# Kernel tuning notes

Measured on AMD Instinct MI355X. Metric: run time of the kernel, lower is better.

## Reference

```python
import jax, jax.numpy as jnp
import numpy as np
import math
from jax import lax


def _conv(x, w, b, stride=1, pad=0, groups=1):
    # x: [B,C,H,W], w: [O, C//groups, kh, kw] (OIHW)
    out = lax.conv_general_dilated(x, w, (stride, stride), [(pad, pad), (pad, pad)],
                                   feature_group_count=groups,
                                   dimension_numbers=('NCHW', 'OIHW', 'NCHW'))
    return out + b.reshape(1, -1, 1, 1)


def _shared_conv(x, k2d, b, stride=1, pad=0):
    # SharedConv: one [k,k] kernel shared across all channels (depthwise), scalar bias
    C = x.shape[1]
    w = jnp.broadcast_to(k2d[None, None], (C, 1) + k2d.shape)
    out = lax.conv_general_dilated(x, w, (stride, stride), [(pad, pad), (pad, pad)],
                                   feature_group_count=C,
                                   dimension_numbers=('NCHW', 'OIHW', 'NCHW'))
    return out + b


def _bn(x, g, b, m, v, eps=1e-5):
    scale = (g / jnp.sqrt(v + eps)).reshape(1, -1, 1, 1)
    return (x - m.reshape(1, -1, 1, 1)) * scale + b.reshape(1, -1, 1, 1)


def _leaky(x, s=0.01):
    return jnp.where(x >= 0, x, s * x)


def _max_leaky(x, t, s):
    # cap values above threshold with leaky slope
    return jnp.where(x <= t, x, t + s * (x - t))


def _min_leaky(x, t, s):
    # cap values below threshold with leaky slope
    return jnp.where(x >= t, x, t + s * (x - t))


def _mode_pool(x, k=11, padding=1):
    # histogram mode pooling: 17 bins over quantized values, stride 1
    xp = jnp.pad(x, ((0, 0), (0, 0), (padding, padding), (padding, padding)))
    bins = jnp.clip(jnp.round(xp * 16.0), 0.0, 16.0).astype(jnp.int32)
    oh = jax.nn.one_hot(bins, 17, dtype=x.dtype)           # [B,C,Hp,Wp,17]
    counts = lax.reduce_window(oh, 0.0, lax.add, (1, 1, k, k, 1), (1, 1, 1, 1, 1), 'VALID')
    return jnp.argmax(counts, axis=-1).astype(x.dtype) / 16.0


def _emphase(x, w, k=11):
    # EmphaseLocal: unsharp-style local emphasis with per-channel learnable scale
    s = lax.reduce_window(x, 0.0, lax.add, (1, 1, k, k), (1, 1, 1, 1), 'SAME')
    avg = s / float(k * k)
    return x + w.reshape(1, -1, 1, 1) * (x - avg)


def setup_inputs() -> dict:
    key = jax.random.key(0)
    ks = jax.random.split(key, 20)
    f32 = jnp.float32
    B, Cin, H, W = 2, 3, 512, 512
    C2 = 64  # half_out_channels * 2
    return {
        'x': jax.random.uniform(ks[0], (B, Cin, H, W), f32),
        'w1': jax.random.normal(ks[1], (C2, Cin, 1, 1), f32) * 0.1,
        'b1': jax.random.normal(ks[2], (C2,), f32) * 0.05,
        'w2': jax.random.normal(ks[3], (C2, 2, 1, 1), f32) * 0.1,  # groups=32
        'b2': jax.random.normal(ks[4], (C2,), f32) * 0.05,
        'down_k': jax.random.normal(ks[5], (3, 3), f32) * 0.1,
        'down_b': jax.random.normal(ks[6], (), f32) * 0.05,
        'ft_gamma': 1.0 + jax.random.normal(ks[7], (C2,), f32) * 0.1,
        'ft_beta': jax.random.normal(ks[8], (C2,), f32) * 0.05,
        'ft_mean': jax.random.normal(ks[9], (C2,), f32) * 0.05,
        'ft_var': jax.random.uniform(ks[10], (C2,), f32, 0.5, 1.5),
        'ft_k': jax.random.normal(ks[11], (1, 1), f32) * 0.5 + 1.0,
        'ft_b': jax.random.normal(ks[12], (), f32) * 0.05,
        'emph_w': jax.random.normal(ks[13], (C2,), f32) * 0.1,
        'interp_k': jax.random.normal(ks[14], (5, 5), f32) * 0.1,
        'interp_b': jax.random.normal(ks[15], (), f32) * 0.05,
        'i_gamma': 1.0 + jax.random.normal(ks[16], (C2,), f32) * 0.1,
        'i_beta': jax.random.normal(ks[17], (C2,), f32) * 0.05,
        'i_mean': jax.random.normal(ks[18], (C2,), f32) * 0.05,
        'i_var': jax.random.uniform(ks[19], (C2,), f32, 0.5, 1.5),
    }


def reference(x, w1, b1, w2, b2, down_k, down_b,
              ft_gamma, ft_beta, ft_mean, ft_var, ft_k, ft_b, emph_w,
              interp_k, interp_b, i_gamma, i_beta, i_mean, i_var):
    B, _, H, W = x.shape
    C2 = w1.shape[0]
    # prepare: ColorDownsample(16) -> ModePool2d(11,1,1) -> 1x1 conv -> MaxLeakyReLU -> grouped 1x1 conv -> MinLeakyReLU
    xd = jnp.round(x * 255.0 / 16.0) * 16.0 / 256.0
    h = _mode_pool(xd, k=11, padding=1)                 # [B,Cin,H-8,W-8]
    h = _max_leaky(_conv(h, w1, b1), 0.1, 0.01)
    groups = C2 // w2.shape[1]
    d = _min_leaky(_conv(h, w2, b2, groups=groups), 0.1, 0.01)
    score = jnp.zeros((B, C2, H, W), x.dtype)
    n = math.floor(math.log(min(d.shape[2], d.shape[3]), 3))
    for _ in range(n):
        # downgrade: shared 3x3 stride-3 conv + leaky
        d = _leaky(_shared_conv(d, down_k, down_b, stride=3, pad=1))
        # zoom back to full resolution, then interpolate branch (shared 5x5 conv + BN + leaky)
        z = jax.image.resize(d, (B, C2, H, W), method='bilinear')
        z = _bn(_shared_conv(z, interp_k, interp_b, pad=2), i_gamma, i_beta, i_mean, i_var)
        score = score + _leaky(z)
    # ft applied 3 times with shared weights: BN -> shared 1x1 conv -> EmphaseLocal
    for _ in range(3):
        s = _bn(score, ft_gamma, ft_beta, ft_mean, ft_var)
        s = _shared_conv(s, ft_k, ft_b)
        score = _emphase(s, emph_w, k=11)
    return score
```

## Files before the change

### kernel.cpp

```cpp
#include <hip/hip_runtime.h>

#define NB 2
#define CIN 3
#define HH 512
#define WW 512
#define C2 64
#define HM 504

typedef float v2f  __attribute__((ext_vector_type(2)));
typedef float v2fu __attribute__((ext_vector_type(2), aligned(4)));

__global__ __launch_bounds__(256) void k_mode(const float* __restrict__ x,
                                              unsigned char* __restrict__ hmode) {
  __shared__ unsigned char tile[26 * 26];
  int bc  = blockIdx.z;
  int ty0 = blockIdx.y * 16, tx0 = blockIdx.x * 16;
  const float* src = x + (size_t)bc * HH * WW;
  for (int i = threadIdx.x; i < 26 * 26; i += 256) {
    int r = i / 26, cl = i % 26;
    int Y = ty0 + r, X = tx0 + cl;
    unsigned char v = 0;
    if (Y >= 1 && Y <= HH && X >= 1 && X <= WW) {
      float val = src[(Y - 1) * WW + (X - 1)];
      float q = rintf((val * 255.0f) / 16.0f);
      q = fminf(fmaxf(q, 0.0f), 16.0f);
      v = (unsigned char)(int)q;
    }
    tile[i] = v;
  }
  __syncthreads();
  int ty = threadIdx.x >> 4, tx = threadIdx.x & 15;
  int oy = ty0 + ty, ox = tx0 + tx;
  if (oy >= HM || ox >= HM) return;
  unsigned long long w0 = 0, w1 = 0, w2 = 0;
  for (int dy = 0; dy < 11; dy++) {
    #pragma unroll
    for (int dx = 0; dx < 11; dx++) {
      int b = tile[(ty + dy) * 26 + tx + dx];
      unsigned long long inc = 1ull << ((b & 7) * 8);
      if (b < 8) w0 += inc;
      else if (b < 16) w1 += inc;
      else w2 += inc;
    }
  }
  int best = -1, bestb = 0;
  #pragma unroll
  for (int b = 0; b < 17; b++) {
    int cnt;
    if (b < 8)       cnt = (int)((w0 >> (b * 8)) & 0xff);
    else if (b < 16) cnt = (int)((w1 >> ((b - 8) * 8)) & 0xff);
    else             cnt = (int)(w2 & 0xff);
    if (cnt > best) { best = cnt; bestb = b; }
  }
  hmode[bc * HM * HM + oy * HM + ox] = (unsigned char)bestb;
}

__global__ __launch_bounds__(256) void k_prepare(const unsigned char* __restrict__ hmode,
                                                 const float* __restrict__ w1,
                                                 const float* __restrict__ b1,
                                                 const float* __restrict__ w2,
                                                 const float* __restrict__ b2,
                                                 const float* __restrict__ down_k,
                                                 const float* __restrict__ down_b,
                                                 float* __restrict__ d1) {
  int bc = blockIdx.y;
  int b  = bc >> 6;
  int c  = bc & 63;
  int pix = blockIdx.x * 256 + threadIdx.x;
  if (pix >= 168 * 168) return;
  int oy = pix / 168, ox = pix % 168;
  int c0 = (c >> 1) << 1;
  float w1a0 = w1[c0 * 3], w1a1 = w1[c0 * 3 + 1], w1a2 = w1[c0 * 3 + 2], b1a = b1[c0];
  float w1b0 = w1[(c0 + 1) * 3], w1b1 = w1[(c0 + 1) * 3 + 1], w1b2 = w1[(c0 + 1) * 3 + 2], b1b = b1[c0 + 1];
  float w2a = w2[c * 2], w2b = w2[c * 2 + 1], b2c = b2[c];
  float kb = *down_b;
  const unsigned char* h0p = hmode + (b * 3 + 0) * HM * HM;
  const unsigned char* h1p = hmode + (b * 3 + 1) * HM * HM;
  const unsigned char* h2p = hmode + (b * 3 + 2) * HM * HM;
  float acc = 0.0f;
  #pragma unroll
  for (int ky = 0; ky < 3; ky++) {
    int y = 3 * oy - 1 + ky;
    if (y < 0 || y >= HM) continue;
    #pragma unroll
    for (int kx = 0; kx < 3; kx++) {
      int xx = 3 * ox - 1 + kx;
      if (xx < 0 || xx >= HM) continue;
      int o = y * HM + xx;
      float hh0 = h0p[o] * (1.0f / 16.0f);
      float hh1 = h1p[o] * (1.0f / 16.0f);
      float hh2 = h2p[o] * (1.0f / 16.0f);
      float a0 = w1a0 * hh0 + w1a1 * hh1 + w1a2 * hh2 + b1a;
      float a1 = w1b0 * hh0 + w1b1 * hh1 + w1b2 * hh2 + b1b;
      a0 = (a0 <= 0.1f) ? a0 : 0.1f + 0.01f * (a0 - 0.1f);
      a1 = (a1 <= 0.1f) ? a1 : 0.1f + 0.01f * (a1 - 0.1f);
      float v = w2a * a0 + w2b * a1 + b2c;
      v = (v >= 0.1f) ? v : 0.1f + 0.01f * (v - 0.1f);
      acc += down_k[ky * 3 + kx] * v;
    }
  }
  float r = acc + kb;
  r = (r >= 0.0f) ? r : 0.01f * r;
  d1[bc * 168 * 168 + pix] = r;
}

__global__ __launch_bounds__(256) void k_down(const float* __restrict__ din,
                                              float* __restrict__ dout,
                                              const float* __restrict__ down_k,
                                              const float* __restrict__ down_b,
                                              int S, int So) {
  int bc = blockIdx.y;
  int pix = blockIdx.x * 256 + threadIdx.x;
  if (pix >= So * So) return;
  int oy = pix / So, ox = pix % So;
  const float* p = din + bc * S * S;
  float acc = 0.0f;
  #pragma unroll
  for (int ky = 0; ky < 3; ky++) {
    int y = 3 * oy - 1 + ky;
    if (y < 0 || y >= S) continue;
    #pragma unroll
    for (int kx = 0; kx < 3; kx++) {
      int xx = 3 * ox - 1 + kx;
      if (xx < 0 || xx >= S) continue;
      acc += down_k[ky * 3 + kx] * p[y * S + xx];
    }
  }
  float r = acc + *down_b;
  r = (r >= 0.0f) ? r : 0.01f * r;
  dout[bc * So * So + pix] = r;
}

__global__ __launch_bounds__(256) void k_lut(float2* __restrict__ lutpk) {
  int idx = blockIdx.x * 256 + threadIdx.x;
  if (idx >= 5 * 512) return;
  int lvl = idx >> 9, Y = idx & 511;
  const int Ls[5] = {168, 56, 19, 7, 3};
  int L = Ls[lvl];
  float f = (Y + 0.5f) * ((float)L / 512.0f) - 0.5f;
  f = fminf(fmaxf(f, 0.0f), (float)(L - 1));
  int y0 = (int)f;
  float w = f - (float)y0;
  lutpk[idx] = make_float2(__int_as_float(y0), w);
}

__global__ __launch_bounds__(256, 4) void k_score(const float* __restrict__ d1,
                                                  const float* __restrict__ d2,
                                                  const float* __restrict__ d3,
                                                  const float* __restrict__ d4,
                                                  const float* __restrict__ d5,
                                                  const float2* __restrict__ lutpk,
                                                  const float* __restrict__ interp_k,
                                                  const float* __restrict__ interp_b,
                                                  const float* __restrict__ i_gamma,
                                                  const float* __restrict__ i_beta,
                                                  const float* __restrict__ i_mean,
                                                  const float* __restrict__ i_var,
                                                  float* __restrict__ score) {
  __shared__ float xrow[24 * 68];
  __shared__ float kap[64 * 20];
  __shared__ int   abase[64];

  int bc = blockIdx.y;
  int c  = bc & 63;
  int tile = blockIdx.x;
  int tyi = tile >> 3, txi = tile & 7;
  int ty0 = tyi * 64, tx0 = txi * 64;
  float K[25];
  #pragma unroll
  for (int i = 0; i < 25; i++)
    K[i] = __int_as_float(__builtin_amdgcn_readfirstlane(__float_as_int(interp_k[i])));
  float ib  = __int_as_float(__builtin_amdgcn_readfirstlane(__float_as_int(*interp_b)));
  float isc = i_gamma[c] * rsqrtf(i_var[c] + 1e-5f);
  float ibe = i_beta[c] - i_mean[c] * isc;
  int tid = threadIdx.x;
  int oyl = (tid >> 4) << 2, oxl = (tid & 15) << 2;
  float acc[4][4];
  #pragma unroll
  for (int i = 0; i < 4; i++)
    #pragma unroll
    for (int j = 0; j < 4; j++) acc[i][j] = 0.0f;

  const float* dls[5] = {d1, d2, d3, d4, d5};
  const int Ls[5]  = {168, 56, 19, 7, 3};
  const int RLs[5] = {24, 10, 5, 3, 3};

  auto fillLevel = [&](int l) {
    int L = Ls[l], RR = RLs[l];
    const float* dp = dls[l] + bc * L * L;
    const float2* lp = lutpk + (l << 9);
    int Ylo = max(ty0 - 2, 0);
    int r0 = __float_as_int(lp[Ylo].x);
    {
      int y = tid >> 2, rr = tid & 3;
      int Y = ty0 + y;
      float kv0 = 0.0f, kv1 = 0.0f, kv2 = 0.0f, kv3 = 0.0f, kv4 = 0.0f;
      int ab = -1;
      #pragma unroll
      for (int ky = 0; ky < 5; ky++) {
        int yy = Y + ky - 2;
        if (yy >= 0 && yy < 512) {
          float2 pk = lp[yy];
          int a0 = __float_as_int(pk.x);
          float wv = pk.y;
          if (ab < 0) ab = a0;
          float cf = 0.0f;
          if (a0 - ab == rr)     cf += 1.0f - wv;
          if (a0 + 1 - ab == rr) cf += wv;
          kv0 += cf * K[ky * 5 + 0];
          kv1 += cf * K[ky * 5 + 1];
          kv2 += cf * K[ky * 5 + 2];
          kv3 += cf * K[ky * 5 + 3];
          kv4 += cf * K[ky * 5 + 4];
        }
      }
      float* kp = &kap[y * 20 + rr * 5];
      kp[0] = kv0; kp[1] = kv1; kp[2] = kv2; kp[3] = kv3; kp[4] = kv4;
      if (rr == 0) abase[y] = ab - r0;
    }
    for (int i = tid; i < RR * 68; i += 256) {
      int r = i / 68, xx = i - r * 68;
      int X = tx0 - 2 + xx;
      float v = 0.0f;
      if (X >= 0 && X < 512) {
        float2 pk = lp[X];
        int ix = __float_as_int(pk.x);
        float wx = pk.y;
        int gr = min(r0 + r, L - 1);
        const float* rp = dp + gr * L + ix;
        float v0 = rp[0], v1 = rp[1];
        v = v0 + wx * (v1 - v0);
      }
      xrow[r * 68 + xx] = v;
    }
  };

  auto convAcc = [&](int rspan, int rlim) {
    #pragma unroll
    for (int i = 0; i < 4; i++) {
      int y = oyl + i;
      int ab = abase[y];
      float t0 = 0.0f, t1 = 0.0f, t2v = 0.0f, t3 = 0.0f;
      for (int rr = 0; rr < rspan; rr++) {
        int row = min(ab + rr, rlim);
        const float* xp = &xrow[row * 68 + oxl];
        float4 A = *(const float4*)xp;
        float4 B = *(const float4*)(xp + 4);
        const float* kp = &kap[y * 20 + rr * 5];
        float k0 = kp[0], k1 = kp[1], k2 = kp[2], k3 = kp[3], k4 = kp[4];
        t0  += k0 * A.x + k1 * A.y + k2 * A.z + k3 * A.w + k4 * B.x;
        t1  += k0 * A.y + k1 * A.z + k2 * A.w + k3 * B.x + k4 * B.y;
        t2v += k0 * A.z + k1 * A.w + k2 * B.x + k3 * B.y + k4 * B.z;
        t3  += k0 * A.w + k1 * B.x + k2 * B.y + k3 * B.z + k4 * B.w;
      }
      float tv[4] = {t0, t1, t2v, t3};
      #pragma unroll
      for (int j = 0; j < 4; j++) {
        float v = (tv[j] + ib) * isc + ibe;
        v = (v >= 0.0f) ? v : 0.01f * v;
        acc[i][j] += v;
      }
    }
  };

  #pragma unroll 1
  for (int l = 0; l < 5; l++) {
    if (l) __syncthreads();
    fillLevel(l);
    __syncthreads();
    if (l == 0) convAcc(4, RLs[0] - 1);
    else        convAcc(3, RLs[l] - 1);
  }

  float* op = score + bc * 512 * 512;
  #pragma unroll
  for (int i = 0; i < 4; i++) {
    int Y = ty0 + oyl + i;
    float4 vv = make_float4(acc[i][0], acc[i][1], acc[i][2], acc[i][3]);
    *(float4*)(op + Y * 512 + tx0 + oxl) = vv;
  }
}

__global__ __launch_bounds__(256, 2) void k_ft_pipe(const float* __restrict__ s_in,
                                                    float* __restrict__ s_out,
                                                    const float* __restrict__ ft_gamma,
                                                    const float* __restrict__ ft_beta,
                                                    const float* __restrict__ ft_mean,
                                                    const float* __restrict__ ft_var,
                                                    const float* __restrict__ ft_k,
                                                    const float* __restrict__ ft_b,
                                                    const float* __restrict__ emph_w) {
  __shared__ float ring2[12 * 512];
  __shared__ float ring3[12 * 512];
  __shared__ float brow1[528];
  __shared__ float brow2[528];
  __shared__ float brow3[528];

  const int bc = blockIdx.y;
  const int c  = bc & 63;
  const int R0 = blockIdx.x << 7;
  const int mstart = R0 - 15;

  const float sc  = ft_gamma[c] * rsqrtf(ft_var[c] + 1e-5f);
  const float fk = *ft_k, fb = *ft_b;
  const float Aff = sc * fk;
  const float Cc  = (ft_beta[c] - ft_mean[c] * sc) * fk + fb;
  const float w   = emph_w[c];
  const float opw = 1.0f + w;
  const float okw = w * (1.0f / 121.0f);

  const int tid = threadIdx.x;
  const int x0  = tid << 1;

  const float* sp = s_in + ((size_t)bc << 18) + x0;
  float*       op = s_out + ((size_t)bc << 18) + x0;

  if (tid < 12) {
    int p = (tid < 6) ? tid : (512 + tid);
    brow1[p] = 0.0f; brow2[p] = 0.0f; brow3[p] = 0.0f;
  }

  auto ldraw = [&](int row) -> v2f {
    int rc = min(max(row, 0), 511);
    return *(const v2f*)(sp + ((size_t)rc << 9));
  };

  auto rowsum = [&](const float* b) -> v2f {
    const float* p = b + x0;
    v2f w0 = *(const v2f*)(p);
    v2f w1 = *(const v2f*)(p + 2);
    v2f w2 = *(const v2f*)(p + 4);
    v2f w3 = *(const v2f*)(p + 6);
    v2f w4 = *(const v2f*)(p + 8);
    v2f w5 = *(const v2f*)(p + 10);
    v2f w6 = *(const v2f*)(p + 12);
    float smid = ((w1.x + w1.y) + (w2.x + w2.y)) +
                 ((w3.x + w3.y) + (w4.x + w4.y)) + (w5.x + w5.y);
    v2f r;
    r.x = smid + w0.y;
    r.y = smid + w6.x;
    return r;
  };

  v2f cs1 = (v2f)0.0f, cs2 = (v2f)0.0f, cs3 = (v2f)0.0f;
  v2f out1p = (v2f)0.0f, out2p = (v2f)0.0f;

  int m = mstart;
  v2f gf = ldraw(m);
  v2f go = ldraw(m - 11);
  v2f gc = ldraw(m - 5);
  int sw = 0;

  #pragma unroll 1
  for (int i = 0; i < 160; ++i, ++m) {
    v2f gf_n = ldraw(m + 1);
    v2f go_n = ldraw(m - 10);
    v2f gc_n = ldraw(m - 4);

    int swn = (sw + 1 == 12) ? 0 : sw + 1;
    int swc = (sw + 7 >= 12) ? sw - 5 : sw + 7;

    {
      v2f u1f = (m >= 0 && m < 512) ? (gf * Aff + Cc) : (v2f)0.0f;
      int r = m - 11;
      v2f u1o = (r >= mstart && r >= 0 && r < 512) ? (go * Aff + Cc) : (v2f)0.0f;
      cs1 += u1f - u1o;
      *(v2f*)(brow1 + 6 + x0) = cs1;
    }
    {
      v2f u2s = out1p * Aff + Cc;
      *(v2f*)(ring2 + sw * 512 + x0) = u2s;
      int rf = m - 6;
      v2f u2f = (rf >= 0 && rf < 512) ? u2s : (v2f)0.0f;
      int r = m - 17;
      v2f u2or = *(const v2f*)(ring2 + swn * 512 + x0);
      v2f u2o = (r >= mstart - 6 && r >= 0 && r < 512) ? u2or : (v2f)0.0f;
      cs2 += u2f - u2o;
      *(v2f*)(brow2 + 6 + x0) = cs2;
    }
    {
      v2f u3s = out2p * Aff + Cc;
      *(v2f*)(ring3 + sw * 512 + x0) = u3s;
      int rf = m - 12;
      v2f u3f = (rf >= 0 && rf < 512) ? u3s : (v2f)0.0f;
      int r = m - 23;
      v2f u3or = *(const v2f*)(ring3 + swn * 512 + x0);
      v2f u3o = (r >= mstart - 12 && r >= 0 && r < 512) ? u3or : (v2f)0.0f;
      cs3 += u3f - u3o;
      *(v2f*)(brow3 + 6 + x0) = cs3;
    }
    __syncthreads();
    {
      int rc1 = m - 5;
      v2f u1c = (rc1 >= 0 && rc1 < 512) ? (gc * Aff + Cc) : (v2f)0.0f;
      v2f B1 = rowsum(brow1);
      out1p = u1c * opw - B1 * okw;
    }
    {
      int rc2 = m - 11;
      v2f u2cr = *(const v2f*)(ring2 + swc * 512 + x0);
      v2f u2c = (rc2 >= mstart - 6 && rc2 >= 0 && rc2 < 512) ? u2cr : (v2f)0.0f;
      v2f B2 = rowsum(brow2);
      out2p = u2c * opw - B2 * okw;
    }
    {
      int rc3 = m - 17;
      v2f u3cr = *(const v2f*)(ring3 + swc * 512 + x0);
      v2f u3c = (rc3 >= mstart - 12 && rc3 >= 0 && rc3 < 512) ? u3cr : (v2f)0.0f;
      v2f B3 = rowsum(brow3);
      v2f o3 = u3c * opw - B3 * okw;
      if (i >= 32)
        *(v2f*)(op + ((size_t)(m - 17) << 9)) = o3;
    }
    __syncthreads();
    gf = gf_n; go = go_n; gc = gc_n;
    sw = swn;
  }
}

extern "C" void kernel_launch(void* const* d_in, const int* in_sizes, int n_in,
                              void* d_out, int out_size, void* d_ws, size_t ws_size,
                              hipStream_t stream) {
  const float* x        = (const float*)d_in[0];
  const float* w1       = (const float*)d_in[1];
  const float* b1       = (const float*)d_in[2];
  const float* w2       = (const float*)d_in[3];
  const float* b2       = (const float*)d_in[4];
  const float* down_k   = (const float*)d_in[5];
  const float* down_b   = (const float*)d_in[6];
  const float* ft_gamma = (const float*)d_in[7];
  const float* ft_beta  = (const float*)d_in[8];
  const float* ft_mean  = (const float*)d_in[9];
  const float* ft_var   = (const float*)d_in[10];
  const float* ft_k     = (const float*)d_in[11];
  const float* ft_b     = (const float*)d_in[12];
  const float* emph_w   = (const float*)d_in[13];
  const float* interp_k = (const float*)d_in[14];
  const float* interp_b = (const float*)d_in[15];
  const float* i_gamma  = (const float*)d_in[16];
  const float* i_beta   = (const float*)d_in[17];
  const float* i_mean   = (const float*)d_in[18];
  const float* i_var    = (const float*)d_in[19];
  float* out = (float*)d_out;

  char* ws = (char*)d_ws;
  size_t off = 0;
  auto alloc = [&](size_t bytes) { size_t r = off; off += (bytes + 255) & ~(size_t)255; return r; };
  unsigned char* hmode = (unsigned char*)(ws + alloc((size_t)NB * CIN * HM * HM));
  float* d1 = (float*)(ws + alloc((size_t)NB * C2 * 168 * 168 * 4));
  float* d2 = (float*)(ws + alloc((size_t)NB * C2 * 56 * 56 * 4));
  float* d3 = (float*)(ws + alloc((size_t)NB * C2 * 19 * 19 * 4));
  float* d4 = (float*)(ws + alloc((size_t)NB * C2 * 7 * 7 * 4));
  float* d5 = (float*)(ws + alloc((size_t)NB * C2 * 3 * 3 * 4));
  float* s0 = (float*)(ws + alloc((size_t)NB * C2 * 512 * 512 * 4));
  float2* lutpk = (float2*)(ws + alloc((size_t)5 * 512 * 8));

  k_mode<<<dim3(32, 32, NB * CIN), 256, 0, stream>>>(x, hmode);
  k_lut<<<10, 256, 0, stream>>>(lutpk);
  k_prepare<<<dim3((168 * 168 + 255) / 256, NB * C2), 256, 0, stream>>>(
      hmode, w1, b1, w2, b2, down_k, down_b, d1);
  k_down<<<dim3((56 * 56 + 255) / 256, NB * C2), 256, 0, stream>>>(d1, d2, down_k, down_b, 168, 56);
  k_down<<<dim3((19 * 19 + 255) / 256, NB * C2), 256, 0, stream>>>(d2, d3, down_k, down_b, 56, 19);
  k_down<<<dim3((7 * 7 + 255) / 256, NB * C2), 256, 0, stream>>>(d3, d4, down_k, down_b, 19, 7);
  k_down<<<dim3((3 * 3 + 255) / 256, NB * C2), 256, 0, stream>>>(d4, d5, down_k, down_b, 7, 3);
  k_score<<<dim3(64, NB * C2), 256, 0, stream>>>(d1, d2, d3, d4, d5, lutpk,
                                                 interp_k, interp_b,
                                                 i_gamma, i_beta, i_mean, i_var, s0);
  k_ft_pipe<<<dim3(4, NB * C2), 256, 0, stream>>>(s0, out, ft_gamma, ft_beta, ft_mean,
                                                  ft_var, ft_k, ft_b, emph_w);
}
```

Baseline: 576.6 us.

## Move ft ring buffers to registers and double-buffer row sums to drop a barrier

The fused three-pass ft kernel now keeps its 12-row delay rings in per-thread registers through a 12-way unrolled loop instead of shared memory. The row-sum staging buffers are double-buffered, which removes the second __syncthreads per row, and the forward global load is prefetched two rows ahead. Shared memory use shrinks, so launch bounds ask for 3 blocks per CU. The trade-off is more registers and code size, and the loop now runs 168 iterations instead of 160, with extra iterations that do not store. Register pressure under the higher occupancy target could cause spills.

After: 549.5 us. 4.7% less time.

```diff
diff --git a/kernel.cpp b/kernel.cpp
--- a/kernel.cpp
+++ b/kernel.cpp
@@ -281,7 +281,7 @@
   }
 }
 
-__global__ __launch_bounds__(256, 2) void k_ft_pipe(const float* __restrict__ s_in,
+__global__ __launch_bounds__(256, 3) void k_ft_pipe(const float* __restrict__ s_in,
                                                     float* __restrict__ s_out,
                                                     const float* __restrict__ ft_gamma,
                                                     const float* __restrict__ ft_beta,
@@ -290,11 +290,9 @@
                                                     const float* __restrict__ ft_k,
                                                     const float* __restrict__ ft_b,
                                                     const float* __restrict__ emph_w) {
-  __shared__ float ring2[12 * 512];
-  __shared__ float ring3[12 * 512];
-  __shared__ float brow1[528];
-  __shared__ float brow2[528];
-  __shared__ float brow3[528];
+  __shared__ float brow1[2][524];
+  __shared__ float brow2[2][524];
+  __shared__ float brow3[2][524];
 
   const int bc = blockIdx.y;
   const int c  = bc & 63;
@@ -315,9 +313,11 @@
   const float* sp = s_in + ((size_t)bc << 18) + x0;
   float*       op = s_out + ((size_t)bc << 18) + x0;
 
-  if (tid < 12) {
-    int p = (tid < 6) ? tid : (512 + tid);
-    brow1[p] = 0.0f; brow2[p] = 0.0f; brow3[p] = 0.0f;
+  if (tid < 72) {
+    int a = tid / 24, pb = (tid / 12) & 1, e = tid % 12;
+    int idx = (e < 6) ? e : (512 + e);
+    float* base = (a == 0) ? &brow1[pb][0] : (a == 1) ? &brow2[pb][0] : &brow3[pb][0];
+    base[idx] = 0.0f;
   }
 
   auto ldraw = [&](int row) -> v2f {
@@ -345,76 +345,81 @@
   v2f cs1 = (v2f)0.0f, cs2 = (v2f)0.0f, cs3 = (v2f)0.0f;
   v2f out1p = (v2f)0.0f, out2p = (v2f)0.0f;
 
-  int m = mstart;
-  v2f gf = ldraw(m);
-  v2f go = ldraw(m - 11);
-  v2f gc = ldraw(m - 5);
-  int sw = 0;
+  v2f r2[12], r3[12];
+  #pragma unroll
+  for (int k = 0; k < 12; k++) { r2[k] = (v2f)0.0f; r3[k] = (v2f)0.0f; }
+
+  v2f gf  = ldraw(mstart);
+  v2f gfa = ldraw(mstart + 1);
+  v2f go  = ldraw(mstart - 11);
+  v2f gc  = ldraw(mstart - 5);
 
   #pragma unroll 1
-  for (int i = 0; i < 160; ++i, ++m) {
-    v2f gf_n = ldraw(m + 1);
-    v2f go_n = ldraw(m - 10);
-    v2f gc_n = ldraw(m - 4);
-
-    int swn = (sw + 1 == 12) ? 0 : sw + 1;
-    int swc = (sw + 7 >= 12) ? sw - 5 : sw + 7;
-
-    {
-      v2f u1f = (m >= 0 && m < 512) ? (gf * Aff + Cc) : (v2f)0.0f;
-      int r = m - 11;
-      v2f u1o = (r >= mstart && r >= 0 && r < 512) ? (go * Aff + Cc) : (v2f)0.0f;
-      cs1 += u1f - u1o;
-      *(v2f*)(brow1 + 6 + x0) = cs1;
-    }
-    {
-      v2f u2s = out1p * Aff + Cc;
-      *(v2f*)(ring2 + sw * 512 + x0) = u2s;
-      int rf = m - 6;
-      v2f u2f = (rf >= 0 && rf < 512) ? u2s : (v2f)0.0f;
-      int r = m - 17;
-      v2f u2or = *(const v2f*)(ring2 + swn * 512 + x0);
-      v2f u2o = (r >= mstart - 6 && r >= 0 && r < 512) ? u2or : (v2f)0.0f;
-      cs2 += u2f - u2o;
-      *(v2f*)(brow2 + 6 + x0) = cs2;
-    }
-    {
-      v2f u3s = out2p * Aff + Cc;
-      *(v2f*)(ring3 + sw * 512 + x0) = u3s;
-      int rf = m - 12;
-      v2f u3f = (rf >= 0 && rf < 512) ? u3s : (v2f)0.0f;
-      int r = m - 23;
-      v2f u3or = *(const v2f*)(ring3 + swn * 512 + x0);
-      v2f u3o = (r >= mstart - 12 && r >= 0 && r < 512) ? u3or : (v2f)0.0f;
-      cs3 += u3f - u3o;
-      *(v2f*)(brow3 + 6 + x0) = cs3;
-    }
-    __syncthreads();
-    {
-      int rc1 = m - 5;
-      v2f u1c = (rc1 >= 0 && rc1 < 512) ? (gc * Aff + Cc) : (v2f)0.0f;
-      v2f B1 = rowsum(brow1);
-      out1p = u1c * opw - B1 * okw;
-    }
-    {
-      int rc2 = m - 11;
-      v2f u2cr = *(const v2f*)(ring2 + swc * 512 + x0);
-      v2f u2c = (rc2 >= mstart - 6 && rc2 >= 0 && rc2 < 512) ? u2cr : (v2f)0.0f;
-      v2f B2 = rowsum(brow2);
-      out2p = u2c * opw - B2 * okw;
-    }
-    {
-      int rc3 = m - 17;
-      v2f u3cr = *(const v2f*)(ring3 + swc * 512 + x0);
-      v2f u3c = (rc3 >= mstart - 12 && rc3 >= 0 && rc3 < 512) ? u3cr : (v2f)0.0f;
-      v2f B3 = rowsum(brow3);
-      v2f o3 = u3c * opw - B3 * okw;
-      if (i >= 32)
-        *(v2f*)(op + ((size_t)(m - 17) << 9)) = o3;
-    }
-    __syncthreads();
-    gf = gf_n; go = go_n; gc = gc_n;
-    sw = swn;
+  for (int ii = 0; ii < 14; ++ii) {
+    #pragma unroll
+    for (int j = 0; j < 12; ++j) {
+      const int i = ii * 12 + j;
+      const int m = mstart + i;
+      v2f gf_n2 = ldraw(m + 2);
+      v2f go_n  = ldraw(m - 10);
+      v2f gc_n  = ldraw(m - 4);
+
+      const int p = j & 1;
+
+      {
+        v2f u1f = (m >= 0 && m < 512) ? (gf * Aff + Cc) : (v2f)0.0f;
+        int r = m - 11;
+        v2f u1o = (r >= mstart && r >= 0 && r < 512) ? (go * Aff + Cc) : (v2f)0.0f;
+        cs1 += u1f - u1o;
+        *(v2f*)(&brow1[p][6 + x0]) = cs1;
+      }
+      {
+        v2f u2s = out1p * Aff + Cc;
+        v2f u2or = r2[(j + 1) % 12];
+        r2[j] = u2s;
+        int rf = m - 6;
+        v2f u2f = (rf >= 0 && rf < 512) ? u2s : (v2f)0.0f;
+        int r = m - 17;
+        v2f u2o = (r >= mstart - 6 && r >= 0 && r < 512) ? u2or : (v2f)0.0f;
+        cs2 += u2f - u2o;
+        *(v2f*)(&brow2[p][6 + x0]) = cs2;
+      }
+      {
+        v2f u3s = out2p * Aff + Cc;
+        v2f u3or = r3[(j + 1) % 12];
+        r3[j] = u3s;
+        int rf = m - 12;
+        v2f u3f = (rf >= 0 && rf < 512) ? u3s : (v2f)0.0f;
+        int r = m - 23;
+        v2f u3o = (r >= mstart - 12 && r >= 0 && r < 512) ? u3or : (v2f)0.0f;
+        cs3 += u3f - u3o;
+        *(v2f*)(&brow3[p][6 + x0]) = cs3;
+      }
+      __syncthreads();
+      {
+        int rc1 = m - 5;
+        v2f u1c = (rc1 >= 0 && rc1 < 512) ? (gc * Aff + Cc) : (v2f)0.0f;
+        v2f B1 = rowsum(&brow1[p][0]);
+        out1p = u1c * opw - B1 * okw;
+      }
+      {
+        int rc2 = m - 11;
+        v2f u2cr = r2[(j + 7) % 12];
+        v2f u2c = (rc2 >= mstart - 6 && rc2 >= 0 && rc2 < 512) ? u2cr : (v2f)0.0f;
+        v2f B2 = rowsum(&brow2[p][0]);
+        out2p = u2c * opw - B2 * okw;
+      }
+      {
+        int rc3 = m - 17;
+        v2f u3cr = r3[(j + 7) % 12];
+        v2f u3c = (rc3 >= mstart - 12 && rc3 >= 0 && rc3 < 512) ? u3cr : (v2f)0.0f;
+        v2f B3 = rowsum(&brow3[p][0]);
+        v2f o3 = u3c * opw - B3 * okw;
+        if (i >= 32 && i < 160)
+          *(v2f*)(op + ((size_t)(m - 17) << 9)) = o3;
+      }
+      gf = gfa; gfa = gf_n2; go = go_n; gc = gc_n;
+    }
   }
 }
 
```
